# Performance work log

Hardware: AMD Instinct MI355X
Metric: run time of the kernel (lower is better)

## Reference

```python
import jax, jax.numpy as jnp
import numpy as np

OUT = 7          # output_size
SR = 2           # sampling_ratio
SCALES = (0.25, 0.125, 0.0625, 0.03125)
K_MIN, K_MAX = 2, 5   # -log2(scales[0]), -log2(scales[-1])
CANON_SCALE, CANON_LVL, EPS = 224.0, 4.0, 1e-6


def _roi_align_level(feat, b_idx, boxes, scale):
    """ROIAlign (maskrcnn-benchmark, non-aligned) of all boxes on one level.
    feat: [B,C,H,W], b_idx: [N] int, boxes: [N,4] xyxy in image coords.
    Returns [N,C,OUT,OUT]."""
    N = boxes.shape[0]
    H, W = feat.shape[2], feat.shape[3]
    x1 = boxes[:, 0] * scale
    y1 = boxes[:, 1] * scale
    x2 = boxes[:, 2] * scale
    y2 = boxes[:, 3] * scale
    roi_w = jnp.maximum(x2 - x1, 1.0)
    roi_h = jnp.maximum(y2 - y1, 1.0)
    bin_w = roi_w / OUT
    bin_h = roi_h / OUT
    # sample positions inside each bin, in bin units: [OUT*SR]
    sub = (jnp.arange(SR, dtype=feat.dtype) + 0.5) / SR
    grid1d = (jnp.arange(OUT, dtype=feat.dtype)[:, None] + sub[None, :]).reshape(-1)
    ys = y1[:, None] + bin_h[:, None] * grid1d[None, :]   # [N, OUT*SR]
    xs = x1[:, None] + bin_w[:, None] * grid1d[None, :]   # [N, OUT*SR]
    K = OUT * SR
    Yf = jnp.broadcast_to(ys[:, :, None], (N, K, K)).reshape(N, K * K)
    Xf = jnp.broadcast_to(xs[:, None, :], (N, K, K)).reshape(N, K * K)
    valid = (Yf >= -1.0) & (Yf <= H) & (Xf >= -1.0) & (Xf <= W)
    y = jnp.clip(Yf, 0.0, H - 1)
    x = jnp.clip(Xf, 0.0, W - 1)
    y0 = jnp.floor(y).astype(jnp.int32)
    x0 = jnp.floor(x).astype(jnp.int32)
    y1i = jnp.minimum(y0 + 1, H - 1)
    x1i = jnp.minimum(x0 + 1, W - 1)
    ly = y - y0
    lx = x - x0
    hy = 1.0 - ly
    hx = 1.0 - lx
    b = b_idx[:, None]  # [N,1] broadcasts with [N,K*K]
    def g(yi, xi):
        return feat[b, :, yi, xi]  # [N, K*K, C]
    val = (g(y0, x0) * (hy * hx)[..., None]
           + g(y0, x1i) * (hy * lx)[..., None]
           + g(y1i, x0) * (ly * hx)[..., None]
           + g(y1i, x1i) * (ly * lx)[..., None])
    val = jnp.where(valid[..., None], val, 0.0)
    # [N, OUT, SR, OUT, SR, C] -> average sampling points -> [N, OUT, OUT, C]
    val = val.reshape(N, OUT, SR, OUT, SR, -1).mean(axis=(2, 4))
    return jnp.transpose(val, (0, 3, 1, 2))  # [N, C, OUT, OUT]


def _map_levels(boxes):
    # BoxList.area with TO_REMOVE = 1 (xyxy mode)
    area = (boxes[:, 2] - boxes[:, 0] + 1.0) * (boxes[:, 3] - boxes[:, 1] + 1.0)
    s = jnp.sqrt(area)
    lvl = jnp.floor(CANON_LVL + jnp.log2(s / CANON_SCALE + EPS))
    lvl = jnp.clip(lvl, K_MIN, K_MAX)
    return lvl.astype(jnp.int32) - K_MIN  # 0..3


def setup_inputs() -> dict:
    key = jax.random.key(0)
    ks = jax.random.split(key, 10)
    N = 1024
    H_img, W_img = 800.0, 1216.0
    x1 = jax.random.uniform(ks[0], (N,), minval=0.0, maxval=W_img - 64.0)
    y1 = jax.random.uniform(ks[1], (N,), minval=0.0, maxval=H_img - 64.0)
    w = jax.random.uniform(ks[2], (N,), minval=8.0, maxval=500.0)
    h = jax.random.uniform(ks[3], (N,), minval=8.0, maxval=500.0)
    x2 = jnp.minimum(x1 + w, W_img - 1.0)
    y2 = jnp.minimum(y1 + h, H_img - 1.0)
    boxes = jnp.stack([x1, y1, x2, y2], axis=1).astype(jnp.float32)
    box_batch_idx = jnp.sort(jax.random.randint(ks[4], (N,), 0, 2)).astype(jnp.int32)
    f0 = jax.random.normal(ks[5], (2, 256, 200, 304), dtype=jnp.float32)
    f1 = jax.random.normal(ks[6], (2, 256, 100, 152), dtype=jnp.float32)
    f2 = jax.random.normal(ks[7], (2, 256, 50, 76), dtype=jnp.float32)
    f3 = jax.random.normal(ks[8], (2, 256, 25, 38), dtype=jnp.float32)
    return {"f0": f0, "f1": f1, "f2": f2, "f3": f3,
            "boxes": boxes, "box_batch_idx": box_batch_idx}


def reference(f0, f1, f2, f3, boxes, box_batch_idx):
    feats = (f0, f1, f2, f3)
    levels = _map_levels(boxes)  # [N] in 0..3
    out = None
    for lvl, (feat, scale) in enumerate(zip(feats, SCALES)):
        pooled = _roi_align_level(feat, box_batch_idx, boxes, scale)
        mask = (levels == lvl)[:, None, None, None]
        part = jnp.where(mask, pooled, 0.0)
        out = part if out is None else out + part
    return out  # [N, C, OUT, OUT]
```

## Files before the change

### kernel.cpp

```cpp
#include <hip/hip_runtime.h>
#include <math.h>

#define TILE_F 1792
#define MAXI 7

typedef __attribute__((address_space(3))) void lds_void;
typedef const __attribute__((address_space(1))) void g_void;

__device__ __forceinline__ void dma16(const float* g, float* l) {
  __builtin_amdgcn_global_load_lds((g_void*)g, (lds_void*)l, 16, 0, 0);
}
__device__ __forceinline__ void dma4(const float* g, float* l) {
  __builtin_amdgcn_global_load_lds((g_void*)g, (lds_void*)l, 4, 0, 0);
}

__global__ __launch_bounds__(128) void pooler_kernel(
    const float* __restrict__ f0, const float* __restrict__ f1,
    const float* __restrict__ f2, const float* __restrict__ f3,
    const float* __restrict__ boxes, const int* __restrict__ bidx,
    float* __restrict__ out, int N)
{
  __shared__ __align__(16) float tile[2][TILE_F];
  const int tid  = threadIdx.x;
  const int wave = tid >> 6, lane = tid & 63;
  const int n    = blockIdx.y;
  if (n >= N) return;

  const float bx1 = boxes[4*n+0], by1 = boxes[4*n+1];
  const float bx2 = boxes[4*n+2], by2 = boxes[4*n+3];
  const float area = (bx2 - bx1 + 1.0f) * (by2 - by1 + 1.0f);
  const float s    = sqrtf(area);
  int lvl = (int)floorf(4.0f + log2f(s / 224.0f + 1e-6f));
  lvl = lvl < 2 ? 2 : (lvl > 5 ? 5 : lvl);
  const int li = lvl - 2;

  int H, W; const float* feat; float scale;
  switch (li) {
    case 0:  feat = f0; H = 200; W = 304; scale = 0.25f;    break;
    case 1:  feat = f1; H = 100; W = 152; scale = 0.125f;   break;
    case 2:  feat = f2; H = 50;  W = 76;  scale = 0.0625f;  break;
    default: feat = f3; H = 25;  W = 38;  scale = 0.03125f; break;
  }
  const int b = bidx[n];
  const float x1s = bx1 * scale, y1s = by1 * scale;
  const float roiw = fmaxf(bx2 * scale - x1s, 1.0f);
  const float roih = fmaxf(by2 * scale - y1s, 1.0f);
  const float binw = roiw / 7.0f, binh = roih / 7.0f;
  const float Hm1f = (float)(H - 1), Wm1f = (float)(W - 1);
  const int   Hm1  = H - 1,          Wm1  = W - 1;

  const float yA = fminf(fmaxf(y1s + binh * 0.25f, 0.0f), Hm1f);
  const float yB = fminf(fmaxf(y1s + binh * 6.75f, 0.0f), Hm1f);
  const float xA = fminf(fmaxf(x1s + binw * 0.25f, 0.0f), Wm1f);
  const float xB = fminf(fmaxf(x1s + binw * 6.75f, 0.0f), Wm1f);
  const int y_lo  = (int)yA;
  const int y_hi  = min((int)yB + 1, Hm1);
  const int regH  = y_hi - y_lo + 1;
  const int x_lo4 = ((int)xA) & ~3;
  const int x_hi  = min((int)xB + 1, Wm1);
  const int row4  = ((x_hi - x_lo4 + 4) >> 2);
  const int regW4 = row4 << 2;

  const int bin = (lane < 49) ? lane : 0;
  const int ph = bin / 7, pw = bin - (bin / 7) * 7;
  int   rT[2], rB[2], Cc0[2], Cc1[2];
  float HY[2], LY[2], VY[2], HX[2], LX[2], VX[2];
#pragma unroll
  for (int t = 0; t < 2; ++t) {
    {
      const float g  = (float)ph + 0.25f + 0.5f * (float)t;
      const float Yf = y1s + binh * g;
      VY[t] = (Yf >= -1.0f && Yf <= (float)H) ? 1.0f : 0.0f;
      const float y = fminf(fmaxf(Yf, 0.0f), Hm1f);
      const int  y0 = (int)y;
      LY[t] = y - (float)y0;  HY[t] = 1.0f - LY[t];
      rT[t] = (y0 - y_lo) * regW4;
      rB[t] = (min(y0 + 1, Hm1) - y_lo) * regW4;
    }
    {
      const float g  = (float)pw + 0.25f + 0.5f * (float)t;
      const float Xf = x1s + binw * g;
      VX[t] = (Xf >= -1.0f && Xf <= (float)W) ? 1.0f : 0.0f;
      const float x = fminf(fmaxf(Xf, 0.0f), Wm1f);
      const int  x0 = (int)x;
      LX[t] = x - (float)x0;  HX[t] = 1.0f - LX[t];
      Cc0[t] = x0 - x_lo4;
      Cc1[t] = min(x0 + 1, Wm1) - x_lo4;
    }
  }

  const size_t planeHW = (size_t)H * W;
  const int    cbase   = (blockIdx.x << 5) + (wave << 4);
  const float* plane0  = feat + ((size_t)(b * 256 + cbase)) * planeHW
                              + (size_t)y_lo * W;
  float*       outp    = out + ((size_t)n * 256 + cbase) * 49 + lane;
  float*       myt     = tile[wave];

  if (li != 3) {
    int cnt4 = regH * row4;
    if (cnt4 > TILE_F / 4) cnt4 = TILE_F / 4;
    int soff[MAXI];
#pragma unroll
    for (int i = 0; i < MAXI; ++i) {
      const int u = lane + (i << 6);
      if (u < cnt4) {
        const int r = u / row4;
        const int c = u - r * row4;
        soff[i] = r * W + x_lo4 + (c << 2);
      } else soff[i] = -1;
    }

    for (int cc = 0; cc < 16; ++cc) {
      const float* plane = plane0 + (size_t)cc * planeHW;
      asm volatile("s_waitcnt lgkmcnt(0)" ::: "memory");
#pragma unroll
      for (int i = 0; i < MAXI; ++i)
        if (soff[i] >= 0) dma16(plane + soff[i], myt + (i << 8));
      asm volatile("s_waitcnt vmcnt(0)" ::: "memory");

      if (lane < 49) {
        float acc = 0.0f;
#pragma unroll
        for (int sy = 0; sy < 2; ++sy) {
#pragma unroll
          for (int sx = 0; sx < 2; ++sx) {
            const float w00 = myt[rT[sy] + Cc0[sx]];
            const float w01 = myt[rT[sy] + Cc1[sx]];
            const float w10 = myt[rB[sy] + Cc0[sx]];
            const float w11 = myt[rB[sy] + Cc1[sx]];
            const float bil = HY[sy] * (HX[sx] * w00 + LX[sx] * w01)
                            + LY[sy] * (HX[sx] * w10 + LX[sx] * w11);
            acc += (VY[sy] * VX[sx]) * bil;
          }
        }
        outp[cc * 49] = acc * 0.25f;
      }
    }
  } else {
    int cntS = regH * regW4;
    if (cntS > TILE_F) cntS = TILE_F;

    for (int cc = 0; cc < 16; ++cc) {
      const float* plane = plane0 + (size_t)cc * planeHW;
      asm volatile("s_waitcnt lgkmcnt(0)" ::: "memory");
      for (int k = 0; (k << 6) < cntS; ++k) {
        const int u = (k << 6) + lane;
        if (u < cntS) {
          const int r   = u / regW4;
          const int c   = u - r * regW4;
          const int col = x_lo4 + c;
          if (col <= Wm1)
            dma4(plane + r * W + col, myt + (k << 6));
        }
      }
      asm volatile("s_waitcnt vmcnt(0)" ::: "memory");

      if (lane < 49) {
        float acc = 0.0f;
#pragma unroll
        for (int sy = 0; sy < 2; ++sy) {
#pragma unroll
          for (int sx = 0; sx < 2; ++sx) {
            const float w00 = myt[rT[sy] + Cc0[sx]];
            const float w01 = myt[rT[sy] + Cc1[sx]];
            const float w10 = myt[rB[sy] + Cc0[sx]];
            const float w11 = myt[rB[sy] + Cc1[sx]];
            const float bil = HY[sy] * (HX[sx] * w00 + LX[sx] * w01)
                            + LY[sy] * (HX[sx] * w10 + LX[sx] * w11);
            acc += (VY[sy] * VX[sx]) * bil;
          }
        }
        outp[cc * 49] = acc * 0.25f;
      }
    }
  }
}

extern "C" void kernel_launch(void* const* d_in, const int* in_sizes, int n_in,
                              void* d_out, int out_size, void* d_ws, size_t ws_size,
                              hipStream_t stream) {
  const float* f0    = (const float*)d_in[0];
  const float* f1    = (const float*)d_in[1];
  const float* f2    = (const float*)d_in[2];
  const float* f3    = (const float*)d_in[3];
  const float* boxes = (const float*)d_in[4];
  const int*   bidx  = (const int*)d_in[5];
  const int N = in_sizes[5];
  dim3 grid(8, N);
  pooler_kernel<<<grid, 128, 0, stream>>>(f0, f1, f2, f3, boxes, bidx,
                                          (float*)d_out, N);
}
```

Before: 280.6 us.

## Replace LDS DMA staging with register float2 loads and channel-pair interleaved tile

Drops the global_load_lds DMA path and the separate level-3 path. Each wave now loads float2 pixel pairs for two channels at once through registers and writes them to LDS interleaved, so the bilinear gather reads float2 and produces two channel outputs per LDS access. The 16 bilinear weights, with the 0.25 average and validity folded in, and the LDS addresses are precomputed once per box. The intent is to halve LDS gather instructions and loop trips and to unify the code paths. In exchange it uses more registers for the staged loads, adds a register round trip compared with direct DMA, and clamps addresses when a region overflows the tile.

```diff
diff --git a/kernel.cpp b/kernel.cpp
--- a/kernel.cpp
+++ b/kernel.cpp
@@ -1,18 +1,8 @@
 #include <hip/hip_runtime.h>
 #include <math.h>
 
-#define TILE_F 1792
-#define MAXI 7
-
-typedef __attribute__((address_space(3))) void lds_void;
-typedef const __attribute__((address_space(1))) void g_void;
-
-__device__ __forceinline__ void dma16(const float* g, float* l) {
-  __builtin_amdgcn_global_load_lds((g_void*)g, (lds_void*)l, 16, 0, 0);
-}
-__device__ __forceinline__ void dma4(const float* g, float* l) {
-  __builtin_amdgcn_global_load_lds((g_void*)g, (lds_void*)l, 4, 0, 0);
-}
+#define TILE_PX 1280
+#define MAXS 10
 
 __global__ __launch_bounds__(128) void pooler_kernel(
     const float* __restrict__ f0, const float* __restrict__ f1,
@@ -20,7 +10,7 @@
     const float* __restrict__ boxes, const int* __restrict__ bidx,
     float* __restrict__ out, int N)
 {
-  __shared__ __align__(16) float tile[2][TILE_F];
+  __shared__ __align__(16) float tile[2][TILE_PX * 2];
   const int tid  = threadIdx.x;
   const int wave = tid >> 6, lane = tid & 63;
   const int n    = blockIdx.y;
@@ -53,126 +43,107 @@
   const float yB = fminf(fmaxf(y1s + binh * 6.75f, 0.0f), Hm1f);
   const float xA = fminf(fmaxf(x1s + binw * 0.25f, 0.0f), Wm1f);
   const float xB = fminf(fmaxf(x1s + binw * 6.75f, 0.0f), Wm1f);
-  const int y_lo  = (int)yA;
-  const int y_hi  = min((int)yB + 1, Hm1);
-  const int regH  = y_hi - y_lo + 1;
-  const int x_lo4 = ((int)xA) & ~3;
-  const int x_hi  = min((int)xB + 1, Wm1);
-  const int row4  = ((x_hi - x_lo4 + 4) >> 2);
-  const int regW4 = row4 << 2;
+  const int y_lo = (int)yA;
+  const int y_hi = min((int)yB + 1, Hm1);
+  const int regH = y_hi - y_lo + 1;
+  const int x_lo = ((int)xA) & ~1;
+  const int x_hi = min((int)xB + 1, Wm1);
+  int regW = x_hi - x_lo + 1;
+  regW += (regW & 1);
+  int npx = regH * regW;
+  if (npx > TILE_PX) npx = TILE_PX;
+  const int npair = npx >> 1;
 
   const int bin = (lane < 49) ? lane : 0;
   const int ph = bin / 7, pw = bin - (bin / 7) * 7;
-  int   rT[2], rB[2], Cc0[2], Cc1[2];
-  float HY[2], LY[2], VY[2], HX[2], LX[2], VX[2];
+  int   rT[2], rB[2], c0[2], c1[2];
+  float hy[2], ly[2], vy[2], hx[2], lx[2], vx[2];
 #pragma unroll
   for (int t = 0; t < 2; ++t) {
-    {
-      const float g  = (float)ph + 0.25f + 0.5f * (float)t;
-      const float Yf = y1s + binh * g;
-      VY[t] = (Yf >= -1.0f && Yf <= (float)H) ? 1.0f : 0.0f;
-      const float y = fminf(fmaxf(Yf, 0.0f), Hm1f);
-      const int  y0 = (int)y;
-      LY[t] = y - (float)y0;  HY[t] = 1.0f - LY[t];
-      rT[t] = (y0 - y_lo) * regW4;
-      rB[t] = (min(y0 + 1, Hm1) - y_lo) * regW4;
+    const float gy = (float)ph + 0.25f + 0.5f * (float)t;
+    const float Yf = y1s + binh * gy;
+    vy[t] = (Yf >= -1.0f && Yf <= (float)H) ? 1.0f : 0.0f;
+    const float y  = fminf(fmaxf(Yf, 0.0f), Hm1f);
+    const int  y0  = (int)y;
+    ly[t] = y - (float)y0;  hy[t] = 1.0f - ly[t];
+    rT[t] = y0 - y_lo;
+    rB[t] = min(y0 + 1, Hm1) - y_lo;
+
+    const float gx = (float)pw + 0.25f + 0.5f * (float)t;
+    const float Xf = x1s + binw * gx;
+    vx[t] = (Xf >= -1.0f && Xf <= (float)W) ? 1.0f : 0.0f;
+    const float x  = fminf(fmaxf(Xf, 0.0f), Wm1f);
+    const int  x0  = (int)x;
+    lx[t] = x - (float)x0;  hx[t] = 1.0f - lx[t];
+    c0[t] = x0 - x_lo;
+    c1[t] = min(x0 + 1, Wm1) - x_lo;
+  }
+  float wgt[16]; int ads[16];
+#pragma unroll
+  for (int sy = 0; sy < 2; ++sy)
+#pragma unroll
+    for (int sx = 0; sx < 2; ++sx) {
+      const int   kk   = (sy * 2 + sx) * 4;
+      const float base = vy[sy] * vx[sx] * 0.25f;
+      wgt[kk+0] = hy[sy] * hx[sx] * base;  ads[kk+0] = (rT[sy]*regW + c0[sx]) * 8;
+      wgt[kk+1] = hy[sy] * lx[sx] * base;  ads[kk+1] = (rT[sy]*regW + c1[sx]) * 8;
+      wgt[kk+2] = ly[sy] * hx[sx] * base;  ads[kk+2] = (rB[sy]*regW + c0[sx]) * 8;
+      wgt[kk+3] = ly[sy] * lx[sx] * base;  ads[kk+3] = (rB[sy]*regW + c1[sx]) * 8;
     }
-    {
-      const float g  = (float)pw + 0.25f + 0.5f * (float)t;
-      const float Xf = x1s + binw * g;
-      VX[t] = (Xf >= -1.0f && Xf <= (float)W) ? 1.0f : 0.0f;
-      const float x = fminf(fmaxf(Xf, 0.0f), Wm1f);
-      const int  x0 = (int)x;
-      LX[t] = x - (float)x0;  HX[t] = 1.0f - LX[t];
-      Cc0[t] = x0 - x_lo4;
-      Cc1[t] = min(x0 + 1, Wm1) - x_lo4;
-    }
+#pragma unroll
+  for (int kk = 0; kk < 16; ++kk)
+    ads[kk] = min(ads[kk], (TILE_PX * 2 - 2) * 4);
+
+  int goff[MAXS];
+#pragma unroll
+  for (int s2 = 0; s2 < MAXS; ++s2) {
+    const int pi = lane + (s2 << 6);
+    if (pi < npair) {
+      const int p = pi << 1;
+      const int r = p / regW;
+      goff[s2] = r * W + (p - r * regW);
+    } else goff[s2] = -1;
   }
 
   const size_t planeHW = (size_t)H * W;
   const int    cbase   = (blockIdx.x << 5) + (wave << 4);
-  const float* plane0  = feat + ((size_t)(b * 256 + cbase)) * planeHW
-                              + (size_t)y_lo * W;
-  float*       outp    = out + ((size_t)n * 256 + cbase) * 49 + lane;
-  float*       myt     = tile[wave];
+  const float* pA   = feat + ((size_t)(b * 256 + cbase)) * planeHW
+                           + (size_t)y_lo * W + x_lo;
+  float*       outp = out + ((size_t)n * 256 + cbase) * 49 + lane;
+  float*       myt  = tile[wave];
 
-  if (li != 3) {
-    int cnt4 = regH * row4;
-    if (cnt4 > TILE_F / 4) cnt4 = TILE_F / 4;
-    int soff[MAXI];
+  for (int cc = 0; cc < 8; ++cc) {
+    const float* p0 = pA;
+    const float* p1 = pA + planeHW;
+    float2 va[MAXS], vb[MAXS];
 #pragma unroll
-    for (int i = 0; i < MAXI; ++i) {
-      const int u = lane + (i << 6);
-      if (u < cnt4) {
-        const int r = u / row4;
-        const int c = u - r * row4;
-        soff[i] = r * W + x_lo4 + (c << 2);
-      } else soff[i] = -1;
+    for (int s2 = 0; s2 < MAXS; ++s2)
+      if (goff[s2] >= 0) {
+        va[s2] = *(const float2*)(p0 + goff[s2]);
+        vb[s2] = *(const float2*)(p1 + goff[s2]);
+      }
+#pragma unroll
+    for (int s2 = 0; s2 < MAXS; ++s2)
+      if (goff[s2] >= 0) {
+        const float4 q = make_float4(va[s2].x, vb[s2].x, va[s2].y, vb[s2].y);
+        *(float4*)&myt[(lane + (s2 << 6)) << 2] = q;
+      }
+    __builtin_amdgcn_wave_barrier();
+
+    if (lane < 49) {
+      float a0 = 0.0f, a1 = 0.0f;
+#pragma unroll
+      for (int kk = 0; kk < 16; ++kk) {
+        const float2 v = *(const float2*)((const char*)myt + ads[kk]);
+        a0 = fmaf(wgt[kk], v.x, a0);
+        a1 = fmaf(wgt[kk], v.y, a1);
+      }
+      outp[0]  = a0;
+      outp[49] = a1;
     }
-
-    for (int cc = 0; cc < 16; ++cc) {
-      const float* plane = plane0 + (size_t)cc * planeHW;
-      asm volatile("s_waitcnt lgkmcnt(0)" ::: "memory");
-#pragma unroll
-      for (int i = 0; i < MAXI; ++i)
-        if (soff[i] >= 0) dma16(plane + soff[i], myt + (i << 8));
-      asm volatile("s_waitcnt vmcnt(0)" ::: "memory");
-
-      if (lane < 49) {
-        float acc = 0.0f;
-#pragma unroll
-        for (int sy = 0; sy < 2; ++sy) {
-#pragma unroll
-          for (int sx = 0; sx < 2; ++sx) {
-            const float w00 = myt[rT[sy] + Cc0[sx]];
-            const float w01 = myt[rT[sy] + Cc1[sx]];
-            const float w10 = myt[rB[sy] + Cc0[sx]];
-            const float w11 = myt[rB[sy] + Cc1[sx]];
-            const float bil = HY[sy] * (HX[sx] * w00 + LX[sx] * w01)
-                            + LY[sy] * (HX[sx] * w10 + LX[sx] * w11);
-            acc += (VY[sy] * VX[sx]) * bil;
-          }
-        }
-        outp[cc * 49] = acc * 0.25f;
-      }
-    }
-  } else {
-    int cntS = regH * regW4;
-    if (cntS > TILE_F) cntS = TILE_F;
-
-    for (int cc = 0; cc < 16; ++cc) {
-      const float* plane = plane0 + (size_t)cc * planeHW;
-      asm volatile("s_waitcnt lgkmcnt(0)" ::: "memory");
-      for (int k = 0; (k << 6) < cntS; ++k) {
-        const int u = (k << 6) + lane;
-        if (u < cntS) {
-          const int r   = u / regW4;
-          const int c   = u - r * regW4;
-          const int col = x_lo4 + c;
-          if (col <= Wm1)
-            dma4(plane + r * W + col, myt + (k << 6));
-        }
-      }
-      asm volatile("s_waitcnt vmcnt(0)" ::: "memory");
-
-      if (lane < 49) {
-        float acc = 0.0f;
-#pragma unroll
-        for (int sy = 0; sy < 2; ++sy) {
-#pragma unroll
-          for (int sx = 0; sx < 2; ++sx) {
-            const float w00 = myt[rT[sy] + Cc0[sx]];
-            const float w01 = myt[rT[sy] + Cc1[sx]];
-            const float w10 = myt[rB[sy] + Cc0[sx]];
-            const float w11 = myt[rB[sy] + Cc1[sx]];
-            const float bil = HY[sy] * (HX[sx] * w00 + LX[sx] * w01)
-                            + LY[sy] * (HX[sx] * w10 + LX[sx] * w11);
-            acc += (VY[sy] * VX[sx]) * bil;
-          }
-        }
-        outp[cc * 49] = acc * 0.25f;
-      }
-    }
+    __builtin_amdgcn_wave_barrier();
+    pA   += 2 * planeHW;
+    outp += 98;
   }
 }
 
```

After: 318.1 us. +13.4%, slower.
